# Performance work log

Hardware: AMD Instinct MI355X
Metric: run time of the kernel (lower is better)

The kernel has to match this reference:

```python
import jax, jax.numpy as jnp
import numpy as np

FREQ_THRESHOLD = 0.1


def setup_inputs() -> dict:
    key = jax.random.key(0)
    images = jax.random.uniform(key, (32, 3, 512, 512), dtype=jnp.float32)
    return {"images": images}


def reference(images):
    # images: [B, C, H, W]
    B, C, H, W = images.shape
    gray = jnp.mean(images, axis=1)                      # [B, H, W]
    fft_magnitude = jnp.abs(jnp.fft.fft2(gray))          # [B, H, W]

    # Radial low-frequency mask centered at (H//2, W//2) -- computed once,
    # shared across the batch (replaces the per-pixel Python loop).
    center_h, center_w = H // 2, W // 2
    radius = min(H, W) * FREQ_THRESHOLD
    yy = jnp.arange(H, dtype=jnp.float32)[:, None]
    xx = jnp.arange(W, dtype=jnp.float32)[None, :]
    dist = jnp.sqrt((yy - center_h) ** 2 + (xx - center_w) ** 2)
    low_freq_mask = (dist <= radius).astype(fft_magnitude.dtype)  # [H, W]

    low_freq_energy = jnp.sum(fft_magnitude * low_freq_mask, axis=(1, 2))  # [B]
    total_energy = jnp.sum(fft_magnitude, axis=(1, 2))                     # [B]
    mura_scores = low_freq_energy / total_energy                           # [B]
    return jnp.mean(mura_scores)                                           # scalar
```

## Files before the change

### kernel.cpp

```cpp
#include <hip/hip_runtime.h>
#include <math.h>

#define N 512
#define LOGN 9
#define NPAD(i) ((i) + ((i) >> 5))
#define FSZ 528
#define NCOL 257
#define RAD2 2621.44f
#define SQ2H 0.70710678f

__device__ __forceinline__ void dft8(float (&xr)[8], float (&xi)[8]) {
    float e0r = xr[0] + xr[4], e0i = xi[0] + xi[4];
    float e1r = xr[0] - xr[4], e1i = xi[0] - xi[4];
    float e2r = xr[2] + xr[6], e2i = xi[2] + xi[6];
    float e3r = xr[2] - xr[6], e3i = xi[2] - xi[6];
    float E0r = e0r + e2r, E0i = e0i + e2i;
    float E2r = e0r - e2r, E2i = e0i - e2i;
    float E1r = e1r + e3i, E1i = e1i - e3r;
    float E3r = e1r - e3i, E3i = e1i + e3r;
    float o0r = xr[1] + xr[5], o0i = xi[1] + xi[5];
    float o1r = xr[1] - xr[5], o1i = xi[1] - xi[5];
    float o2r = xr[3] + xr[7], o2i = xi[3] + xi[7];
    float o3r = xr[3] - xr[7], o3i = xi[3] - xi[7];
    float O0r = o0r + o2r, O0i = o0i + o2i;
    float O2r = o0r - o2r, O2i = o0i - o2i;
    float O1r = o1r + o3i, O1i = o1i - o3r;
    float O3r = o1r - o3i, O3i = o1i + o3r;
    float t1r = SQ2H * (O1r + O1i), t1i = SQ2H * (O1i - O1r);
    float t2r = O2i,                t2i = -O2r;
    float t3r = SQ2H * (O3i - O3r), t3i = -SQ2H * (O3r + O3i);
    xr[0] = E0r + O0r; xi[0] = E0i + O0i;
    xr[4] = E0r - O0r; xi[4] = E0i - O0i;
    xr[1] = E1r + t1r; xi[1] = E1i + t1i;
    xr[5] = E1r - t1r; xi[5] = E1i - t1i;
    xr[2] = E2r + t2r; xi[2] = E2i + t2i;
    xr[6] = E2r - t2r; xi[6] = E2i - t2i;
    xr[3] = E3r + t3r; xi[3] = E3i + t3i;
    xr[7] = E3r - t3r; xi[7] = E3i - t3i;
}

__device__ __forceinline__ void fft512_regs(float (&zr)[8], float (&zi)[8],
                                            int l) {
    dft8(zr, zi);
    float a = (-2.0f * (float)M_PI / 512.0f) * (float)l;
    float w1r, w1i;
    __sincosf(a, &w1i, &w1r);
    float wr = w1r, wi = w1i;
#pragma unroll
    for (int k = 1; k < 8; ++k) {
        float tr = zr[k] * wr - zi[k] * wi;
        float ti = zr[k] * wi + zi[k] * wr;
        zr[k] = tr; zi[k] = ti;
        float nr = wr * w1r - wi * w1i;
        float ni = wr * w1i + wi * w1r;
        wr = nr; wi = ni;
    }
#pragma unroll
    for (int half = 32; half >= 1; half >>= 1) {
        int j = l & (half - 1);
        float ang = (-(float)M_PI / (float)half) * (float)j;
        float swr, swi;
        __sincosf(ang, &swi, &swr);
        bool up = (l & half) != 0;
        float sgn = up ? -1.0f : 1.0f;
        float wsr = up ? swr : 1.0f;
        float wsi = up ? swi : 0.0f;
#pragma unroll
        for (int k = 0; k < 8; ++k) {
            float pr = __shfl_xor(zr[k], half);
            float pi = __shfl_xor(zi[k], half);
            float tr = fmaf(sgn, zr[k], pr);
            float ti = fmaf(sgn, zi[k], pi);
            zr[k] = tr * wsr - ti * wsi;
            zi[k] = tr * wsi + ti * wsr;
        }
    }
}

__global__ __launch_bounds__(512) void k_gray_rowfft(
    const float* __restrict__ img, float2* __restrict__ buf) {
    __shared__ float sr[8][FSZ], si[8][FSZ];
    const int t = threadIdx.x, wv = t >> 6, l = t & 63;
    const int b = blockIdx.y, tile = blockIdx.x;
    const size_t plane = (size_t)N * N;
    const float* base = img + (size_t)b * 3 * plane;
    const int he = tile * 16 + 2 * wv;
    const float* p0 = base + (size_t)he * N;
    const float* p1 = p0 + N;

    float zr[8], zi[8];
#pragma unroll
    for (int j = 0; j < 8; ++j) {
        int w = l + 64 * j;
        zr[j] = (p0[w] + p0[plane + w] + p0[2 * plane + w]) * (1.0f / 3.0f);
        zi[j] = (p1[w] + p1[plane + w] + p1[2 * plane + w]) * (1.0f / 3.0f);
    }

    fft512_regs(zr, zi, l);

    const int rb = __brev((unsigned)l) >> 26;
#pragma unroll
    for (int k = 0; k < 8; ++k) {
        int u = 8 * rb + k;
        sr[wv][NPAD(u)] = zr[k];
        si[wv][NPAD(u)] = zi[k];
    }
    __syncthreads();

    const int h = t & 15, p = h >> 1, odd = h & 1, slot = t >> 4;
    float2* ob = buf + (size_t)b * NCOL * N;
#pragma unroll
    for (int it = 0; it <= 8; ++it) {
        int v = slot + 32 * it;
        if (v < NCOL) {
            int vn = (N - v) & (N - 1);
            float Zr  = sr[p][NPAD(v)],  Zi  = si[p][NPAD(v)];
            float Zr2 = sr[p][NPAD(vn)], Zi2 = si[p][NPAD(vn)];
            float Fr, Fi;
            if (!odd) { Fr = 0.5f * (Zr + Zr2); Fi = 0.5f * (Zi - Zi2); }
            else      { Fr = 0.5f * (Zi + Zi2); Fi = 0.5f * (Zr2 - Zr); }
            ob[(size_t)v * N + tile * 16 + h] = make_float2(Fr, Fi);
        }
    }
}

__global__ __launch_bounds__(256) void k_colfft_reduce(
    const float2* __restrict__ buf, float* __restrict__ acc) {
    __shared__ float red[8];
    const int t = threadIdx.x, wv = t >> 6, l = t & 63;
    const int b = blockIdx.y;
    const int v = blockIdx.x * 4 + wv;
    const int vv = v > 256 ? 256 : v;

    const float2* col = buf + ((size_t)b * NCOL + vv) * N;
    float zr[8], zi[8];
#pragma unroll
    for (int j = 0; j < 8; ++j) {
        float2 z = col[64 * j + l];
        zr[j] = z.x; zi[j] = z.y;
    }

    fft512_regs(zr, zi, l);

    const float wcol = (v == 0 || v == 256) ? 1.0f : (v < 256 ? 2.0f : 0.0f);
    const float dx = (float)(vv - 256);
    const float dx2 = dx * dx;
    const int rb = __brev((unsigned)l) >> 26;
    float msum = 0.0f, tsum = 0.0f;
#pragma unroll
    for (int k = 0; k < 8; ++k) {
        int u = 8 * rb + k;
        float mag = sqrtf(zr[k] * zr[k] + zi[k] * zi[k]);
        tsum += mag;
        float dy = (float)(u - 256);
        if (dy * dy + dx2 <= RAD2) msum += mag;
    }
    msum *= wcol; tsum *= wcol;
#pragma unroll
    for (int off = 32; off > 0; off >>= 1) {
        msum += __shfl_down(msum, off);
        tsum += __shfl_down(tsum, off);
    }
    if (l == 0) { red[wv * 2] = msum; red[wv * 2 + 1] = tsum; }
    __syncthreads();
    if (t == 0) {
        atomicAdd(&acc[b * 2 + 0], red[0] + red[2] + red[4] + red[6]);
        atomicAdd(&acc[b * 2 + 1], red[1] + red[3] + red[5] + red[7]);
    }
}

__global__ void k_final(const float* __restrict__ acc,
                        float* __restrict__ out) {
    int t = threadIdx.x;
    float r = 0.0f;
    if (t < 32) r = acc[t * 2 + 0] / acc[t * 2 + 1];
#pragma unroll
    for (int off = 32; off > 0; off >>= 1) r += __shfl_down(r, off);
    if (t == 0) out[0] = r * (1.0f / 32.0f);
}

extern "C" void kernel_launch(void* const* d_in, const int* in_sizes, int n_in,
                              void* d_out, int out_size, void* d_ws,
                              size_t ws_size, hipStream_t stream) {
    const float* img = (const float*)d_in[0];
    float* out = (float*)d_out;

    float2* buf = (float2*)d_ws;
    const size_t buf_bytes = (size_t)32 * NCOL * N * sizeof(float2);
    float* acc = (float*)((char*)d_ws + buf_bytes);

    hipMemsetAsync(acc, 0, 64 * sizeof(float), stream);

    dim3 g1(N / 16, 32);
    k_gray_rowfft<<<g1, 512, 0, stream>>>(img, buf);

    dim3 g2((NCOL + 3) / 4, 32);
    k_colfft_reduce<<<g2, 256, 0, stream>>>(buf, acc);

    k_final<<<1, 64, 0, stream>>>(acc, out);
}
```

Before: 186.8 us.

## Restructure FFT as decimation-in-frequency with per-thread-contiguous inputs and vectorized IO

The 512-point register FFT is reordered so that each thread holds 8 contiguous input elements. The cross-lane butterflies now run first, then the twiddles, then a local radix-8 DFT. This lets both kernels load their inputs with float4 instead of strided scalars, and the row kernel writes its even/odd split results as float4 pairs. Twiddles now come from the hardware sin/cos builtins, which take revolutions as input, replacing __sincosf and the recurrence. The cost is lower twiddle precision and a changed LDS padding size.

```diff
diff --git a/kernel.cpp b/kernel.cpp
--- a/kernel.cpp
+++ b/kernel.cpp
@@ -2,9 +2,8 @@
 #include <math.h>
 
 #define N 512
-#define LOGN 9
 #define NPAD(i) ((i) + ((i) >> 5))
-#define FSZ 528
+#define FSZ 532
 #define NCOL 257
 #define RAD2 2621.44f
 #define SQ2H 0.70710678f
@@ -41,40 +40,37 @@
 
 __device__ __forceinline__ void fft512_regs(float (&zr)[8], float (&zi)[8],
                                             int l) {
-    dft8(zr, zi);
-    float a = (-2.0f * (float)M_PI / 512.0f) * (float)l;
-    float w1r, w1i;
-    __sincosf(a, &w1i, &w1r);
-    float wr = w1r, wi = w1i;
-#pragma unroll
-    for (int k = 1; k < 8; ++k) {
-        float tr = zr[k] * wr - zi[k] * wi;
-        float ti = zr[k] * wi + zi[k] * wr;
-        zr[k] = tr; zi[k] = ti;
-        float nr = wr * w1r - wi * w1i;
-        float ni = wr * w1i + wi * w1r;
-        wr = nr; wi = ni;
-    }
 #pragma unroll
     for (int half = 32; half >= 1; half >>= 1) {
-        int j = l & (half - 1);
-        float ang = (-(float)M_PI / (float)half) * (float)j;
-        float swr, swi;
-        __sincosf(ang, &swi, &swr);
-        bool up = (l & half) != 0;
-        float sgn = up ? -1.0f : 1.0f;
-        float wsr = up ? swr : 1.0f;
-        float wsi = up ? swi : 0.0f;
+        const int j = l & (half - 1);
+        const float f = (float)j * (0.5f / (float)half);
+        const float c = __builtin_amdgcn_cosf(f);
+        const float s = __builtin_amdgcn_sinf(f);
+        const bool up = (l & half) != 0;
+        const float sgn = up ? -1.0f : 1.0f;
+        const float wc  = up ? c : 1.0f;
+        const float ws  = up ? s : 0.0f;
 #pragma unroll
         for (int k = 0; k < 8; ++k) {
             float pr = __shfl_xor(zr[k], half);
             float pi = __shfl_xor(zi[k], half);
             float tr = fmaf(sgn, zr[k], pr);
             float ti = fmaf(sgn, zi[k], pi);
-            zr[k] = tr * wsr - ti * wsi;
-            zi[k] = tr * wsi + ti * wsr;
+            zr[k] = tr * wc + ti * ws;
+            zi[k] = ti * wc - tr * ws;
         }
     }
+    const int w = __brev((unsigned)l) >> 26;
+#pragma unroll
+    for (int k = 1; k < 8; ++k) {
+        const float f = (float)(k * w) * (1.0f / 512.0f);
+        const float c = __builtin_amdgcn_cosf(f);
+        const float s = __builtin_amdgcn_sinf(f);
+        float tr = zr[k] * c + zi[k] * s;
+        float ti = zi[k] * c - zr[k] * s;
+        zr[k] = tr; zi[k] = ti;
+    }
+    dft8(zr, zi);
 }
 
 __global__ __launch_bounds__(512) void k_gray_rowfft(
@@ -88,38 +84,58 @@
     const float* p0 = base + (size_t)he * N;
     const float* p1 = p0 + N;
 
+    const float4* c0e = (const float4*)(p0);
+    const float4* c1e = (const float4*)(p0 + plane);
+    const float4* c2e = (const float4*)(p0 + 2 * plane);
+    const float4* c0o = (const float4*)(p1);
+    const float4* c1o = (const float4*)(p1 + plane);
+    const float4* c2o = (const float4*)(p1 + 2 * plane);
+
     float zr[8], zi[8];
-#pragma unroll
-    for (int j = 0; j < 8; ++j) {
-        int w = l + 64 * j;
-        zr[j] = (p0[w] + p0[plane + w] + p0[2 * plane + w]) * (1.0f / 3.0f);
-        zi[j] = (p1[w] + p1[plane + w] + p1[2 * plane + w]) * (1.0f / 3.0f);
+    const float inv3 = 1.0f / 3.0f;
+#pragma unroll
+    for (int q = 0; q < 2; ++q) {
+        int idx = 2 * l + q;
+        float4 a = c0e[idx], bb = c1e[idx], c = c2e[idx];
+        float4 d = c0o[idx], e = c1o[idx], g = c2o[idx];
+        zr[4 * q + 0] = (a.x + bb.x + c.x) * inv3;
+        zr[4 * q + 1] = (a.y + bb.y + c.y) * inv3;
+        zr[4 * q + 2] = (a.z + bb.z + c.z) * inv3;
+        zr[4 * q + 3] = (a.w + bb.w + c.w) * inv3;
+        zi[4 * q + 0] = (d.x + e.x + g.x) * inv3;
+        zi[4 * q + 1] = (d.y + e.y + g.y) * inv3;
+        zi[4 * q + 2] = (d.z + e.z + g.z) * inv3;
+        zi[4 * q + 3] = (d.w + e.w + g.w) * inv3;
     }
 
     fft512_regs(zr, zi, l);
 
-    const int rb = __brev((unsigned)l) >> 26;
+    const int w = __brev((unsigned)l) >> 26;
 #pragma unroll
     for (int k = 0; k < 8; ++k) {
-        int u = 8 * rb + k;
+        int u = w + 64 * k;
         sr[wv][NPAD(u)] = zr[k];
         si[wv][NPAD(u)] = zi[k];
     }
     __syncthreads();
 
-    const int h = t & 15, p = h >> 1, odd = h & 1, slot = t >> 4;
+    const int p = t & 7;
+    const int h2 = 2 * p;
+    const int slot = t >> 3;
     float2* ob = buf + (size_t)b * NCOL * N;
 #pragma unroll
-    for (int it = 0; it <= 8; ++it) {
-        int v = slot + 32 * it;
+    for (int it = 0; it < 5; ++it) {
+        int v = slot + 64 * it;
         if (v < NCOL) {
             int vn = (N - v) & (N - 1);
             float Zr  = sr[p][NPAD(v)],  Zi  = si[p][NPAD(v)];
             float Zr2 = sr[p][NPAD(vn)], Zi2 = si[p][NPAD(vn)];
-            float Fr, Fi;
-            if (!odd) { Fr = 0.5f * (Zr + Zr2); Fi = 0.5f * (Zi - Zi2); }
-            else      { Fr = 0.5f * (Zi + Zi2); Fi = 0.5f * (Zr2 - Zr); }
-            ob[(size_t)v * N + tile * 16 + h] = make_float2(Fr, Fi);
+            float4 o;
+            o.x = 0.5f * (Zr + Zr2);
+            o.y = 0.5f * (Zi - Zi2);
+            o.z = 0.5f * (Zi + Zi2);
+            o.w = 0.5f * (Zr2 - Zr);
+            *(float4*)(&ob[(size_t)v * N + tile * 16 + h2]) = o;
         }
     }
 }
@@ -132,12 +148,13 @@
     const int v = blockIdx.x * 4 + wv;
     const int vv = v > 256 ? 256 : v;
 
-    const float2* col = buf + ((size_t)b * NCOL + vv) * N;
+    const float4* col = (const float4*)(buf + ((size_t)b * NCOL + vv) * N);
     float zr[8], zi[8];
 #pragma unroll
-    for (int j = 0; j < 8; ++j) {
-        float2 z = col[64 * j + l];
-        zr[j] = z.x; zi[j] = z.y;
+    for (int q = 0; q < 4; ++q) {
+        float4 z = col[4 * l + q];
+        zr[2 * q]     = z.x; zi[2 * q]     = z.y;
+        zr[2 * q + 1] = z.z; zi[2 * q + 1] = z.w;
     }
 
     fft512_regs(zr, zi, l);
@@ -145,11 +162,11 @@
     const float wcol = (v == 0 || v == 256) ? 1.0f : (v < 256 ? 2.0f : 0.0f);
     const float dx = (float)(vv - 256);
     const float dx2 = dx * dx;
-    const int rb = __brev((unsigned)l) >> 26;
+    const int w = __brev((unsigned)l) >> 26;
     float msum = 0.0f, tsum = 0.0f;
 #pragma unroll
     for (int k = 0; k < 8; ++k) {
-        int u = 8 * rb + k;
+        int u = w + 64 * k;
         float mag = sqrtf(zr[k] * zr[k] + zi[k] * zi[k]);
         tsum += mag;
         float dy = (float)(u - 256);
```

New measurement: 185.7 us. No clear change (-0.6%).
